# Performance work log

Measured on AMD Instinct MI355X. Metric: run time of the kernel, lower is better.

The kernel has to match this reference:

```python
import jax, jax.numpy as jnp
import numpy as np

B, C, Np, D = 16, 64, 128, 128
HT = 4      # time heads
HS = 4      # space heads (GAT)
F = D       # GAT out_channels
DK = D // 2 # q/k proj dim
TOPK = 8
NEG = -1e30

def ln(x, g, b):
    m = x.mean(-1, keepdims=True)
    v = jnp.mean((x - m) ** 2, axis=-1, keepdims=True)
    return (x - m) / jnp.sqrt(v + 1e-5) * g + b

def setup_inputs() -> dict:
    key = jax.random.key(0)
    ks = jax.random.split(key, 16)
    w = lambda k, s: (jax.random.normal(k, s, jnp.float32) * 0.02)
    return dict(
        H_in=jax.random.normal(ks[0], (B, C, Np, D), jnp.float32),
        static_adj=jax.random.normal(ks[1], (C, C), jnp.float32) * 0.1,
        attn_in_w=w(ks[2], (3 * D, D)), attn_in_b=jnp.zeros((3 * D,), jnp.float32),
        attn_out_w=w(ks[3], (D, D)), attn_out_b=jnp.zeros((D,), jnp.float32),
        ln1_g=jnp.ones((D,), jnp.float32), ln1_b=jnp.zeros((D,), jnp.float32),
        ln2_g=jnp.ones((D,), jnp.float32), ln2_b=jnp.zeros((D,), jnp.float32),
        ff1_w=w(ks[4], (4 * D, D)), ff1_b=jnp.zeros((4 * D,), jnp.float32),
        ff2_w=w(ks[5], (D, 4 * D)), ff2_b=jnp.zeros((D,), jnp.float32),
        tnorm_g=jnp.ones((D,), jnp.float32), tnorm_b=jnp.zeros((D,), jnp.float32),
        q_w=w(ks[6], (DK, D)), q_b=jnp.zeros((DK,), jnp.float32),
        k_w=w(ks[7], (DK, D)), k_b=jnp.zeros((DK,), jnp.float32),
        gat_w=w(ks[8], (HS, F, D)),
        gat_att_src=w(ks[9], (HS, F)), gat_att_dst=w(ks[10], (HS, F)),
        gat_bias=jnp.zeros((D,), jnp.float32),
        snorm_g=jnp.ones((D,), jnp.float32), snorm_b=jnp.zeros((D,), jnp.float32),
    )

def _forward(H_in, static_adj, attn_in_w, attn_in_b, attn_out_w, attn_out_b,
             ln1_g, ln1_b, ln2_g, ln2_b, ff1_w, ff1_b, ff2_w, ff2_b,
             tnorm_g, tnorm_b, q_w, q_b, k_w, k_b,
             gat_w, gat_att_src, gat_att_dst, gat_bias, snorm_g, snorm_b):
    dh = D // HT
    # ---- temporal transformer encoder layer (norm_first) on [B*C, Np, D]
    x0 = H_in.reshape(B * C, Np, D)
    h = ln(x0, ln1_g, ln1_b)
    qkv = h @ attn_in_w.T + attn_in_b
    q, k, v = jnp.split(qkv, 3, axis=-1)
    q = q.reshape(-1, Np, HT, dh).transpose(0, 2, 1, 3)
    k = k.reshape(-1, Np, HT, dh).transpose(0, 2, 1, 3)
    v = v.reshape(-1, Np, HT, dh).transpose(0, 2, 1, 3)
    att = jax.nn.softmax(jnp.einsum('nhqd,nhkd->nhqk', q, k) / jnp.sqrt(jnp.float32(dh)), axis=-1)
    o = jnp.einsum('nhqk,nhkd->nhqd', att, v).transpose(0, 2, 1, 3).reshape(-1, Np, D)
    x = x0 + (o @ attn_out_w.T + attn_out_b)
    h2 = ln(x, ln2_g, ln2_b)
    x = x + jax.nn.relu(h2 @ ff1_w.T + ff1_b) @ ff2_w.T + ff2_b
    H_temp = ln(x0 + x, tnorm_g, tnorm_b).reshape(B, C, Np, D)
    # ---- dynamic adjacency from temporal summary
    Hs = H_temp.mean(axis=2)                              # [B,C,D]
    q2 = Hs @ q_w.T + q_b
    k2 = Hs @ k_w.T + k_b
    sim = jnp.einsum('bcd,bed->bce', q2, k2) * (DK ** -0.5)
    A = jnp.tanh(sim) + static_adj[None]                  # [B,C,C]
    # ---- top-k edge mask per sample (row r -> its top-k cols, no self loops)
    kk = max(1, min(TOPK, C - 1))
    idx = jax.lax.top_k(A, kk)[1]                         # [B,C,kk]
    mask = jnp.any(jax.nn.one_hot(idx, C, dtype=bool), axis=2)  # [B,C,C]
    mask = mask & (~jnp.eye(C, dtype=bool)) & (A != 0)
    # ---- dense masked GAT over all (B, Np) graphs; src=row, dst=col
    xh = jnp.einsum('bcpd,hfd->bphcf', H_temp, gat_w)     # [B,Np,HS,C,F]
    asrc = jnp.einsum('bphcf,hf->bphc', xh, gat_att_src)
    adst = jnp.einsum('bphcf,hf->bphc', xh, gat_att_dst)
    e = asrc[..., :, None] + adst[..., None, :]           # [B,Np,HS,src,dst]
    e = jnp.where(e > 0, e, 0.2 * e)                      # LeakyReLU(0.2)
    mb = mask[:, None, None, :, :]
    e = jnp.where(mb, e, NEG)
    e = e - e.max(axis=3, keepdims=True)                  # softmax over src per dst
    wgt = jnp.exp(e) * mb
    s = wgt.sum(axis=3, keepdims=True)
    a = wgt / jnp.where(s > 0, s, 1.0)
    out = jnp.einsum('bphst,bphsf->bphtf', a, xh).mean(axis=2) + gat_bias  # [B,Np,C,F]
    out = out.transpose(0, 2, 1, 3)                       # [B,C,Np,D]
    return ln(out + H_temp, snorm_g, snorm_b)

def reference(H_in, static_adj, attn_in_w, attn_in_b, attn_out_w, attn_out_b,
              ln1_g, ln1_b, ln2_g, ln2_b, ff1_w, ff1_b, ff2_w, ff2_b,
              tnorm_g, tnorm_b, q_w, q_b, k_w, k_b,
              gat_w, gat_att_src, gat_att_dst, gat_bias, snorm_g, snorm_b):
    return _forward(H_in, static_adj, attn_in_w, attn_in_b, attn_out_w, attn_out_b,
                    ln1_g, ln1_b, ln2_g, ln2_b, ff1_w, ff1_b, ff2_w, ff2_b,
                    tnorm_g, tnorm_b, q_w, q_b, k_w, k_b,
                    gat_w, gat_att_src, gat_att_dst, gat_bias, snorm_g, snorm_b)
```

## Files before the change

kernel.cpp:

```cpp
#include <hip/hip_runtime.h>
#include <cstdint>


typedef __attribute__((ext_vector_type(8)))  short bf16x8;
typedef __attribute__((ext_vector_type(16))) float f32x16;
#define MFMA32(a, b, c) __builtin_amdgcn_mfma_f32_32x32x16_bf16((a), (b), (c), 0, 0, 0)

__device__ __forceinline__ unsigned short f2bf(float f) {
    unsigned int u = __float_as_uint(f);
    u += 0x7fffu + ((u >> 16) & 1u);
    return (unsigned short)(u >> 16);
}
__device__ __forceinline__ float bf2f(unsigned short u) {
    return __uint_as_float(((unsigned int)u) << 16);
}

__device__ __forceinline__ bf16x8 lds_frag(const unsigned short* p) {
    union { bf16x8 v; ushort4 h[2]; } u;
    u.h[0] = *(const ushort4*)p;
    u.h[1] = *(const ushort4*)(p + 4);
    return u.v;
}
__device__ __forceinline__ bf16x8 gfrag(const unsigned short* p) {
    union { bf16x8 v; uint4 u; } t;
    t.u = *(const uint4*)p;
    return t.v;
}

__device__ __forceinline__ int rowmap(int r, int hl) { return (r & 3) + 8 * (r >> 2) + 4 * hl; }

__global__ void wconv_kernel(const float* __restrict__ wqkv, const float* __restrict__ wout,
                             const float* __restrict__ w1, const float* __restrict__ w2,
                             const float* __restrict__ gw,
                             unsigned short* __restrict__ dst) {
    int i = blockIdx.x * 256 + threadIdx.x;
    float v;
    if (i < 49152)       v = wqkv[i];
    else if (i < 65536)  v = wout[i - 49152];
    else if (i < 131072) v = w1[i - 65536];
    else if (i < 196608) v = w2[i - 131072];
    else                 v = gw[i - 196608];
    dst[i] = f2bf(v);
}

__global__ void wa_kernel(const float* __restrict__ gw, const float* __restrict__ asw,
                          const float* __restrict__ adw,
                          float* __restrict__ waS, float* __restrict__ waD) {
    int t = blockIdx.x * 256 + threadIdx.x;
    int h = t >> 8, d = (t >> 1) & 127, which = t & 1;
    const float* av = which ? adw : asw;
    float s = 0.f;
    for (int f = 0; f < 128; f++) s += av[h * 128 + f] * gw[(h * 128 + f) * 128 + d];
    (which ? waD : waS)[h * 128 + d] = s;
}

__global__ __launch_bounds__(256, 1)
void seq_attn_kernel(const float* __restrict__ Hin,
                     const unsigned short* __restrict__ wqkv_b,
                     const float* __restrict__ bqkv,
                     const float* __restrict__ g1, const float* __restrict__ b1,
                     char* __restrict__ dout) {
    __shared__ unsigned short hb[128][132];
    __shared__ unsigned short qb[128][36];
    __shared__ unsigned short kb[128][36];
    __shared__ unsigned short vT[32][132];
    __shared__ unsigned short Bst[3][32][132];
    __shared__ unsigned short Pb[4][32][132];

    const int n = blockIdx.x;
    const int tid = threadIdx.x;
    const int lane = tid & 63;
    const int wv = tid >> 6;
    const int hl = lane >> 5;
    const int l31 = lane & 31;

    {
        int row = tid >> 1, hf = tid & 1;
        const float* src = Hin + ((long)n * 128 + row) * 128 + hf * 64;
        float xv[64];
        float s = 0.f, qs = 0.f;
#pragma unroll
        for (int i = 0; i < 64; i += 4) {
            float4 t = *(const float4*)(src + i);
            xv[i] = t.x; xv[i+1] = t.y; xv[i+2] = t.z; xv[i+3] = t.w;
        }
#pragma unroll
        for (int i = 0; i < 64; i++) { s += xv[i]; qs += xv[i] * xv[i]; }
        s += __shfl_xor(s, 1); qs += __shfl_xor(qs, 1);
        float mu = s * 0.0078125f;
        float rs = rsqrtf(fmaxf(qs * 0.0078125f - mu * mu, 0.f) + 1e-5f);
#pragma unroll
        for (int i = 0; i < 64; i++) {
            int d = hf * 64 + i;
            hb[row][d] = f2bf((xv[i] - mu) * rs * g1[d] + b1[d]);
        }
    }
    __syncthreads();

    unsigned short* Optr = (unsigned short*)(dout + (long)n * 65536 + 32768);

    for (int h = 0; h < 4; h++) {
        for (int idx = tid; idx < 1536; idx += 256) {
            int mat = idx >> 9;
            int rem = idx & 511;
            int j = rem >> 4, kc = rem & 15;
            const unsigned short* s8 = wqkv_b + ((mat * 128 + h * 32 + j) * 128 + kc * 8);
            ushort4 lo = *(const ushort4*)s8, hi = *(const ushort4*)(s8 + 4);
            unsigned short* d8 = &Bst[mat][j][kc * 8];
            *(ushort4*)d8 = lo; *(ushort4*)(d8 + 4) = hi;
        }
        __syncthreads();

        {
            f32x16 accq, acck, accv;
            float bq = bqkv[      h * 32 + l31];
            float bk = bqkv[128 + h * 32 + l31];
            float bv = bqkv[256 + h * 32 + l31];
#pragma unroll
            for (int r = 0; r < 16; r++) { accq[r] = bq; acck[r] = bk; accv[r] = bv; }
#pragma unroll
            for (int k0 = 0; k0 < 128; k0 += 16) {
                bf16x8 a  = lds_frag(&hb[wv * 32 + l31][k0 + hl * 8]);
                bf16x8 b0 = lds_frag(&Bst[0][l31][k0 + hl * 8]);
                bf16x8 b1f = lds_frag(&Bst[1][l31][k0 + hl * 8]);
                bf16x8 b2f = lds_frag(&Bst[2][l31][k0 + hl * 8]);
                accq = MFMA32(a, b0, accq);
                acck = MFMA32(a, b1f, acck);
                accv = MFMA32(a, b2f, accv);
            }
#pragma unroll
            for (int r = 0; r < 16; r++) {
                int tok = wv * 32 + rowmap(r, hl);
                qb[tok][l31] = f2bf(accq[r]);
                kb[tok][l31] = f2bf(acck[r]);
                vT[l31][tok] = f2bf(accv[r]);
            }
        }
        __syncthreads();

        f32x16 sacc[4];
#pragma unroll
        for (int t = 0; t < 4; t++)
#pragma unroll
            for (int r = 0; r < 16; r++) sacc[t][r] = 0.f;
#pragma unroll
        for (int k0 = 0; k0 < 32; k0 += 16) {
            bf16x8 a = lds_frag(&qb[wv * 32 + l31][k0 + hl * 8]);
#pragma unroll
            for (int t = 0; t < 4; t++) {
                bf16x8 b = lds_frag(&kb[t * 32 + l31][k0 + hl * 8]);
                sacc[t] = MFMA32(a, b, sacc[t]);
            }
        }
        const float scale = 0.17677669529663687f;
#pragma unroll
        for (int r = 0; r < 16; r++) {
            float m0 = fmaxf(fmaxf(sacc[0][r], sacc[1][r]), fmaxf(sacc[2][r], sacc[3][r]));
#pragma unroll
            for (int d = 1; d < 32; d <<= 1) m0 = fmaxf(m0, __shfl_xor(m0, d));
            float ssum = 0.f;
#pragma unroll
            for (int t = 0; t < 4; t++) {
                float e = __expf(scale * (sacc[t][r] - m0));
                sacc[t][r] = e; ssum += e;
            }
#pragma unroll
            for (int d = 1; d < 32; d <<= 1) ssum += __shfl_xor(ssum, d);
            float rinv = 1.f / ssum;
            int row = rowmap(r, hl);
#pragma unroll
            for (int t = 0; t < 4; t++)
                Pb[wv][row][t * 32 + l31] = f2bf(sacc[t][r] * rinv);
        }

        f32x16 oacc;
#pragma unroll
        for (int r = 0; r < 16; r++) oacc[r] = 0.f;
#pragma unroll
        for (int k0 = 0; k0 < 128; k0 += 16) {
            bf16x8 a = lds_frag(&Pb[wv][l31][k0 + hl * 8]);
            bf16x8 b = lds_frag(&vT[l31][k0 + hl * 8]);
            oacc = MFMA32(a, b, oacc);
        }
#pragma unroll
        for (int r = 0; r < 16; r++) {
            int tok = wv * 32 + rowmap(r, hl);
            Optr[tok * 128 + h * 32 + l31] = f2bf(oacc[r]);
        }
        __syncthreads();
    }
}

__global__ __launch_bounds__(256, 1)
void mlp_kernel(const float* __restrict__ Hin,
                const unsigned short* __restrict__ wout_b, const float* __restrict__ bout,
                const float* __restrict__ g2, const float* __restrict__ b2,
                const unsigned short* __restrict__ w1_b, const float* __restrict__ bf1,
                const unsigned short* __restrict__ w2_b, const float* __restrict__ bf2,
                const float* __restrict__ tg, const float* __restrict__ tb,
                char* __restrict__ dout) {
    __shared__ unsigned short Ab[128][132];
    __shared__ unsigned short h2b[128][132];
    __shared__ unsigned short BA[128][132];
    __shared__ unsigned short BB[128][132];

    const int n = blockIdx.x;
    const int tid = threadIdx.x;
    const int lane = tid & 63;
    const int wv = tid >> 6;
    const int hl = lane >> 5;
    const int l31 = lane & 31;

    const unsigned short* Optr = (const unsigned short*)(dout + (long)n * 65536 + 32768);

    for (int idx = tid; idx < 2048; idx += 256) {
        int row = idx >> 4, kc = idx & 15;
        {
            const ushort4* s = (const ushort4*)(Optr + row * 128 + kc * 8);
            unsigned short* d = &Ab[row][kc * 8];
            *(ushort4*)d = s[0]; *(ushort4*)(d + 4) = s[1];
        }
        {
            const ushort4* s = (const ushort4*)(wout_b + row * 128 + kc * 8);
            unsigned short* d = &BA[row][kc * 8];
            *(ushort4*)d = s[0]; *(ushort4*)(d + 4) = s[1];
        }
    }
    __syncthreads();

    f32x16 acc[4];
#pragma unroll
    for (int t = 0; t < 4; t++) {
        float bo = bout[t * 32 + l31];
#pragma unroll
        for (int r = 0; r < 16; r++) {
            int tok = wv * 32 + rowmap(r, hl);
            acc[t][r] = Hin[((long)n * 128 + tok) * 128 + t * 32 + l31] + bo;
        }
    }
#pragma unroll
    for (int k0 = 0; k0 < 128; k0 += 16) {
        bf16x8 a = lds_frag(&Ab[wv * 32 + l31][k0 + hl * 8]);
#pragma unroll
        for (int t = 0; t < 4; t++) {
            bf16x8 b = lds_frag(&BA[t * 32 + l31][k0 + hl * 8]);
            acc[t] = MFMA32(a, b, acc[t]);
        }
    }

#pragma unroll
    for (int r = 0; r < 16; r++) {
        float s = acc[0][r] + acc[1][r] + acc[2][r] + acc[3][r];
#pragma unroll
        for (int d = 1; d < 32; d <<= 1) s += __shfl_xor(s, d);
        float mu = s * 0.0078125f;
        float q = 0.f;
#pragma unroll
        for (int t = 0; t < 4; t++) { float dv = acc[t][r] - mu; q += dv * dv; }
#pragma unroll
        for (int d = 1; d < 32; d <<= 1) q += __shfl_xor(q, d);
        float rs = rsqrtf(q * 0.0078125f + 1e-5f);
        int row = wv * 32 + rowmap(r, hl);
#pragma unroll
        for (int t = 0; t < 4; t++) {
            int col = t * 32 + l31;
            h2b[row][col] = f2bf((acc[t][r] - mu) * rs * g2[col] + b2[col]);
        }
    }

    f32x16 acc2[4];
#pragma unroll
    for (int t = 0; t < 4; t++) {
        float bv = bf2[t * 32 + l31];
#pragma unroll
        for (int r = 0; r < 16; r++) acc2[t][r] = acc[t][r] + bv;
    }

    for (int j = 0; j < 4; j++) {
        __syncthreads();
        for (int idx = tid; idx < 2048; idx += 256) {
            int row = idx >> 4, kc = idx & 15;
            {
                const ushort4* s = (const ushort4*)(w1_b + ((j * 128 + row) * 128 + kc * 8));
                unsigned short* d = &BA[row][kc * 8];
                *(ushort4*)d = s[0]; *(ushort4*)(d + 4) = s[1];
            }
            {
                const ushort4* s = (const ushort4*)(w2_b + (row * 512 + j * 128 + kc * 8));
                unsigned short* d = &BB[row][kc * 8];
                *(ushort4*)d = s[0]; *(ushort4*)(d + 4) = s[1];
            }
        }
        __syncthreads();

        f32x16 racc[4];
#pragma unroll
        for (int t = 0; t < 4; t++) {
            float bv = bf1[j * 128 + t * 32 + l31];
#pragma unroll
            for (int r = 0; r < 16; r++) racc[t][r] = bv;
        }
#pragma unroll
        for (int k0 = 0; k0 < 128; k0 += 16) {
            bf16x8 a = lds_frag(&h2b[wv * 32 + l31][k0 + hl * 8]);
#pragma unroll
            for (int t = 0; t < 4; t++) {
                bf16x8 b = lds_frag(&BA[t * 32 + l31][k0 + hl * 8]);
                racc[t] = MFMA32(a, b, racc[t]);
            }
        }
#pragma unroll
        for (int t = 0; t < 4; t++)
#pragma unroll
            for (int r = 0; r < 16; r++) {
                int row = wv * 32 + rowmap(r, hl);
                Ab[row][t * 32 + l31] = f2bf(fmaxf(racc[t][r], 0.f));
            }

#pragma unroll
        for (int k0 = 0; k0 < 128; k0 += 16) {
            bf16x8 a = lds_frag(&Ab[wv * 32 + l31][k0 + hl * 8]);
#pragma unroll
            for (int t = 0; t < 4; t++) {
                bf16x8 b = lds_frag(&BB[t * 32 + l31][k0 + hl * 8]);
                acc2[t] = MFMA32(a, b, acc2[t]);
            }
        }
    }

#pragma unroll
    for (int t = 0; t < 4; t++)
#pragma unroll
        for (int r = 0; r < 16; r++) {
            int tok = wv * 32 + rowmap(r, hl);
            acc2[t][r] += Hin[((long)n * 128 + tok) * 128 + t * 32 + l31];
        }
    float* outf = (float*)dout + (long)n * 16384;
#pragma unroll
    for (int r = 0; r < 16; r++) {
        float s = acc2[0][r] + acc2[1][r] + acc2[2][r] + acc2[3][r];
#pragma unroll
        for (int d = 1; d < 32; d <<= 1) s += __shfl_xor(s, d);
        float mu = s * 0.0078125f;
        float q = 0.f;
#pragma unroll
        for (int t = 0; t < 4; t++) { float dv = acc2[t][r] - mu; q += dv * dv; }
#pragma unroll
        for (int d = 1; d < 32; d <<= 1) q += __shfl_xor(q, d);
        float rs = rsqrtf(q * 0.0078125f + 1e-5f);
        int tok = wv * 32 + rowmap(r, hl);
#pragma unroll
        for (int t = 0; t < 4; t++) {
            int col = t * 32 + l31;
            outf[tok * 128 + col] = (acc2[t][r] - mu) * rs * tg[col] + tb[col];
        }
    }
}

__global__ void hs_kernel(const float* __restrict__ Htemp, float* __restrict__ Hs) {
    int idx = blockIdx.x * 256 + threadIdx.x;
    int n = idx >> 7, d = idx & 127;
    float s = 0.f;
    for (int p = 0; p < 128; p++) s += Htemp[((long)n * 128 + p) * 128 + d];
    Hs[idx] = s * 0.0078125f;
}

__global__ __launch_bounds__(256)
void graph_kernel(const float* __restrict__ Hs,
                  const float* __restrict__ qw, const float* __restrict__ qb,
                  const float* __restrict__ kw, const float* __restrict__ kb,
                  const float* __restrict__ adj, unsigned long long* __restrict__ masks) {
    __shared__ float q2l[64][65];
    __shared__ float k2l[64][65];
    __shared__ float am[64][65];
    int b = blockIdx.x;
    int tid = threadIdx.x;
    {
        int r = tid & 127, jh = tid >> 7;
        int row = r & 63;
        const float* wmat = (r < 64) ? qw : kw;
        const float* bvec = (r < 64) ? qb : kb;
        const float* src = Hs + (long)(b * 64 + row) * 128;
        for (int jj = 0; jj < 32; jj++) {
            int j = jh * 32 + jj;
            const float* wrow = wmat + (long)j * 128;
            float s0 = 0.f, s1 = 0.f, s2 = 0.f, s3 = 0.f;
#pragma unroll
            for (int d = 0; d < 128; d += 4) {
                s0 += src[d] * wrow[d];     s1 += src[d+1] * wrow[d+1];
                s2 += src[d+2] * wrow[d+2]; s3 += src[d+3] * wrow[d+3];
            }
            float val = ((s0 + s1) + (s2 + s3)) + bvec[j];
            if (r < 64) q2l[row][j] = val; else k2l[row][j] = val;
        }
    }
    __syncthreads();
    {
        int c = tid & 63, eq = tid >> 6;
        for (int ee = 0; ee < 16; ee++) {
            int e = eq * 16 + ee;
            float s0 = 0.f, s1 = 0.f, s2 = 0.f, s3 = 0.f;
#pragma unroll
            for (int j = 0; j < 64; j += 4) {
                s0 += q2l[c][j]   * k2l[e][j];
                s1 += q2l[c][j+1] * k2l[e][j+1];
                s2 += q2l[c][j+2] * k2l[e][j+2];
                s3 += q2l[c][j+3] * k2l[e][j+3];
            }
            float sim = ((s0 + s1) + (s2 + s3)) * 0.125f;
            am[c][e] = tanhf(sim) + adj[c * 64 + e];
        }
    }
    __syncthreads();
    if (tid < 64) {
        int c = tid;
        unsigned long long sel = 0ull;
        for (int it = 0; it < 8; it++) {
            float best = -1e38f; int bi = 0;
            for (int e = 0; e < 64; e++) {
                float v = am[c][e];
                bool ok = (((sel >> e) & 1ull) == 0ull) && (v > best);
                best = ok ? v : best;
                bi = ok ? e : bi;
            }
            sel |= (1ull << bi);
        }
        sel &= ~(1ull << c);
        for (int e = 0; e < 64; e++)
            if (am[c][e] == 0.f) sel &= ~(1ull << e);
        masks[b * 64 + c] = sel;
    }
}

__global__ __launch_bounds__(256, 1)
void gat_kernel(float* __restrict__ Htemp,
                const unsigned short* __restrict__ gwb,
                const float* __restrict__ waS, const float* __restrict__ waD,
                const float* __restrict__ gbias,
                const unsigned long long* __restrict__ masks,
                const float* __restrict__ sg, const float* __restrict__ sb) {
    __shared__ unsigned short Htb[64][132];
    __shared__ double ovl_d[3264];
    __shared__ float asrcF[4][64], adstF[4][64];
    __shared__ float pmax[4][64], psum[4][64];
    __shared__ unsigned long long mk[64];

    unsigned short (*xhT)[68]  = (unsigned short(*)[68])ovl_d;
    unsigned short (*attT)[68] = (unsigned short(*)[68])((char*)ovl_d + 17408);
    float (*part)[8][64]       = (float(*)[8][64])ovl_d;

    const int bp = blockIdx.x;
    const int b = bp >> 7, p = bp & 127;
    const int tid = threadIdx.x;
    const int lane = tid & 63, wv = tid >> 6;
    const int hl = lane >> 5, l31 = lane & 31;
    const int rs = (wv & 1) * 32;
    const int cs = (wv >> 1) * 64;

    {
        int c = tid >> 2, qq = tid & 3;
        const float* src = Htemp + ((long)(b * 64 + c) * 128 + p) * 128 + qq * 32;
#pragma unroll
        for (int k = 0; k < 8; k++) {
            float4 t4 = *(const float4*)(src + 4 * k);
            ushort4 u; u.x = f2bf(t4.x); u.y = f2bf(t4.y); u.z = f2bf(t4.z); u.w = f2bf(t4.w);
            *(ushort4*)&Htb[c][qq * 32 + 4 * k] = u;
        }
    }
    if (tid < 64) mk[tid] = masks[b * 64 + tid];
    __syncthreads();

    {
        int s = lane, q = wv;
        float acc[8];
#pragma unroll
        for (int m = 0; m < 8; m++) acc[m] = 0.f;
        const unsigned int* hp = (const unsigned int*)&Htb[s][q * 32];
#pragma unroll
        for (int d2 = 0; d2 < 16; d2++) {
            unsigned int u = hp[d2];
            float f0 = __uint_as_float(u << 16);
            float f1 = __uint_as_float(u & 0xffff0000u);
            int d = q * 32 + 2 * d2;
#pragma unroll
            for (int h = 0; h < 4; h++) {
                acc[2*h]   += f0 * waS[h * 128 + d] + f1 * waS[h * 128 + d + 1];
                acc[2*h+1] += f0 * waD[h * 128 + d] + f1 * waD[h * 128 + d + 1];
            }
        }
#pragma unroll
        for (int m = 0; m < 8; m++) part[q][m][s] = acc[m];
    }
    __syncthreads();
    for (int o = tid; o < 512; o += 256) {
        int h = o >> 7, rem = o & 127, which = rem >> 6, s = rem & 63;
        int m = h * 2 + which;
        float v = part[0][m][s] + part[1][m][s] + part[2][m][s] + part[3][m][s];
        if (which == 0) asrcF[h][s] = v; else adstF[h][s] = v;
    }
    __syncthreads();

    f32x16 oacc0, oacc1;
#pragma unroll
    for (int r = 0; r < 16; r++) { oacc0[r] = 0.f; oacc1[r] = 0.f; }

    for (int h = 0; h < 4; h++) {
        f32x16 a0, a1;
#pragma unroll
        for (int r = 0; r < 16; r++) { a0[r] = 0.f; a1[r] = 0.f; }
        const unsigned short* gwh = gwb + h * 16384;
#pragma unroll
        for (int k0 = 0; k0 < 128; k0 += 16) {
            bf16x8 af = lds_frag(&Htb[rs + l31][k0 + hl * 8]);
            bf16x8 b0 = gfrag(gwh + (cs + l31) * 128 + k0 + hl * 8);
            bf16x8 b1 = gfrag(gwh + (cs + 32 + l31) * 128 + k0 + hl * 8);
            a0 = MFMA32(af, b0, a0);
            a1 = MFMA32(af, b1, a1);
        }
#pragma unroll
        for (int g = 0; g < 4; g++) {
            ushort4 u0, u1;
            u0.x = f2bf(a0[4*g]);   u0.y = f2bf(a0[4*g+1]);
            u0.z = f2bf(a0[4*g+2]); u0.w = f2bf(a0[4*g+3]);
            u1.x = f2bf(a1[4*g]);   u1.y = f2bf(a1[4*g+1]);
            u1.z = f2bf(a1[4*g+2]); u1.w = f2bf(a1[4*g+3]);
            int so = rs + 4 * hl + 8 * g;
            *(ushort4*)&xhT[cs + l31][so]      = u0;
            *(ushort4*)&xhT[cs + 32 + l31][so] = u1;
        }
        __syncthreads();

        {
            int t = lane;
            float adv = adstF[h][t];
            float ev[16];
            float mx = -1e30f;
#pragma unroll
            for (int i = 0; i < 16; i++) {
                int s = wv * 16 + i;
                float e = asrcF[h][s] + adv;
                e = (e > 0.f) ? e : 0.2f * e;
                ev[i] = e;
                if ((mk[s] >> t) & 1ull) mx = fmaxf(mx, e);
            }
            pmax[wv][t] = mx;
            __syncthreads();
            float M = fmaxf(fmaxf(pmax[0][t], pmax[1][t]), fmaxf(pmax[2][t], pmax[3][t]));
            float sm = 0.f;
#pragma unroll
            for (int i = 0; i < 16; i++) {
                int s = wv * 16 + i;
                float w = ((mk[s] >> t) & 1ull) ? __expf(ev[i] - M) : 0.f;
                ev[i] = w; sm += w;
            }
            psum[wv][t] = sm;
            __syncthreads();
            float S = psum[0][t] + psum[1][t] + psum[2][t] + psum[3][t];
            float rinv = (S > 0.f) ? 1.f / S : 0.f;
#pragma unroll
            for (int g = 0; g < 4; g++) {
                ushort4 u;
                u.x = f2bf(ev[4*g]   * rinv); u.y = f2bf(ev[4*g+1] * rinv);
                u.z = f2bf(ev[4*g+2] * rinv); u.w = f2bf(ev[4*g+3] * rinv);
                *(ushort4*)&attT[t][wv * 16 + 4 * g] = u;
            }
        }
        __syncthreads();

#pragma unroll
        for (int k0 = 0; k0 < 64; k0 += 16) {
            bf16x8 af = lds_frag(&attT[rs + l31][k0 + hl * 8]);
            bf16x8 b0 = lds_frag(&xhT[cs + l31][k0 + hl * 8]);
            bf16x8 b1 = lds_frag(&xhT[cs + 32 + l31][k0 + hl * 8]);
            oacc0 = MFMA32(af, b0, oacc0);
            oacc1 = MFMA32(af, b1, oacc1);
        }
        __syncthreads();
    }

    float gb0 = gbias[cs + l31], gb1 = gbias[cs + 32 + l31];
    float v0[16], v1[16];
#pragma unroll
    for (int r = 0; r < 16; r++) {
        int c = rs + rowmap(r, hl);
        v0[r] = oacc0[r] * 0.25f + gb0 + bf2f(Htb[c][cs + l31]);
        v1[r] = oacc1[r] * 0.25f + gb1 + bf2f(Htb[c][cs + 32 + l31]);
    }
#pragma unroll
    for (int r = 0; r < 16; r++) {
        float s = v0[r] + v1[r];
        float q = v0[r] * v0[r] + v1[r] * v1[r];
#pragma unroll
        for (int d = 1; d < 32; d <<= 1) { s += __shfl_xor(s, d); q += __shfl_xor(q, d); }
        if (l31 == 0) {
            int c = rs + rowmap(r, hl);
            pmax[wv >> 1][c] = s;
            psum[wv >> 1][c] = q;
        }
    }
    __syncthreads();
    float sgv0 = sg[cs + l31], sbv0 = sb[cs + l31];
    float sgv1 = sg[cs + 32 + l31], sbv1 = sb[cs + 32 + l31];
#pragma unroll
    for (int r = 0; r < 16; r++) {
        int c = rs + rowmap(r, hl);
        float sum = pmax[0][c] + pmax[1][c];
        float sq  = psum[0][c] + psum[1][c];
        float mu = sum * 0.0078125f;
        float var = sq * 0.0078125f - mu * mu;
        float rsd = rsqrtf(fmaxf(var, 0.f) + 1e-5f);
        float* orow = Htemp + ((long)(b * 64 + c) * 128 + p) * 128;
        orow[cs + l31]      = (v0[r] - mu) * rsd * sgv0 + sbv0;
        orow[cs + 32 + l31] = (v1[r] - mu) * rsd * sgv1 + sbv1;
    }
}

extern "C" void kernel_launch(void* const* d_in, const int* in_sizes, int n_in,
                              void* d_out, int out_size, void* d_ws, size_t ws_size,
                              hipStream_t stream) {
    const float* Hin        = (const float*)d_in[0];
    const float* static_adj = (const float*)d_in[1];
    const float* attn_in_w  = (const float*)d_in[2];
    const float* attn_in_b  = (const float*)d_in[3];
    const float* attn_out_w = (const float*)d_in[4];
    const float* attn_out_b = (const float*)d_in[5];
    const float* ln1_g      = (const float*)d_in[6];
    const float* ln1_b      = (const float*)d_in[7];
    const float* ln2_g      = (const float*)d_in[8];
    const float* ln2_b      = (const float*)d_in[9];
    const float* ff1_w      = (const float*)d_in[10];
    const float* ff1_b      = (const float*)d_in[11];
    const float* ff2_w      = (const float*)d_in[12];
    const float* ff2_b      = (const float*)d_in[13];
    const float* tnorm_g    = (const float*)d_in[14];
    const float* tnorm_b    = (const float*)d_in[15];
    const float* q_w        = (const float*)d_in[16];
    const float* q_b        = (const float*)d_in[17];
    const float* k_w        = (const float*)d_in[18];
    const float* k_b        = (const float*)d_in[19];
    const float* gat_w      = (const float*)d_in[20];
    const float* gat_att_src= (const float*)d_in[21];
    const float* gat_att_dst= (const float*)d_in[22];
    const float* gat_bias   = (const float*)d_in[23];
    const float* snorm_g    = (const float*)d_in[24];
    const float* snorm_b    = (const float*)d_in[25];

    char* out = (char*)d_out;
    char* ws = (char*)d_ws;
    unsigned short* wb = (unsigned short*)ws;
    const unsigned short* wqkv_b = wb;
    const unsigned short* wout_b = wb + 49152;
    const unsigned short* w1_b   = wb + 65536;
    const unsigned short* w2_b   = wb + 131072;
    const unsigned short* gw_b   = wb + 196608;
    unsigned long long* masks = (unsigned long long*)(ws + 524288);
    float* Hs  = (float*)(ws + 532480);
    float* waS = (float*)(ws + 1056768);
    float* waD = (float*)(ws + 1058816);

    hipLaunchKernelGGL(wconv_kernel, dim3(1024), dim3(256), 0, stream,
                       attn_in_w, attn_out_w, ff1_w, ff2_w, gat_w, wb);
    hipLaunchKernelGGL(wa_kernel, dim3(4), dim3(256), 0, stream,
                       gat_w, gat_att_src, gat_att_dst, waS, waD);
    hipLaunchKernelGGL(seq_attn_kernel, dim3(1024), dim3(256), 0, stream,
                       Hin, wqkv_b, attn_in_b, ln1_g, ln1_b, out);
    hipLaunchKernelGGL(mlp_kernel, dim3(1024), dim3(256), 0, stream,
                       Hin, wout_b, attn_out_b, ln2_g, ln2_b,
                       w1_b, ff1_b, w2_b, ff2_b, tnorm_g, tnorm_b, out);
    hipLaunchKernelGGL(hs_kernel, dim3(512), dim3(256), 0, stream, (float*)out, Hs);
    hipLaunchKernelGGL(graph_kernel, dim3(16), dim3(256), 0, stream,
                       Hs, q_w, q_b, k_w, k_b, static_adj, masks);
    hipLaunchKernelGGL(gat_kernel, dim3(2048), dim3(256), 0, stream,
                       (float*)out, gw_b, waS, waD, gat_bias,
                       masks, snorm_g, snorm_b);
}
```

Measured before the change: 657.4 us.

## Fuse temporal attention and MLP into one kernel with global-read weight fragments

Result: faster. 622.9 us (-5.2%).

```diff
diff --git a/kernel.cpp b/kernel.cpp
--- a/kernel.cpp
+++ b/kernel.cpp
@@ -54,18 +54,23 @@
     (which ? waD : waS)[h * 128 + d] = s;
 }
 
-__global__ __launch_bounds__(256, 1)
-void seq_attn_kernel(const float* __restrict__ Hin,
-                     const unsigned short* __restrict__ wqkv_b,
-                     const float* __restrict__ bqkv,
+__global__ __launch_bounds__(256, 2)
+void temporal_kernel(const float* __restrict__ Hin,
+                     const unsigned short* __restrict__ wqkv_b, const float* __restrict__ bqkv,
+                     const unsigned short* __restrict__ wout_b, const float* __restrict__ bout,
                      const float* __restrict__ g1, const float* __restrict__ b1,
-                     char* __restrict__ dout) {
-    __shared__ unsigned short hb[128][132];
-    __shared__ unsigned short qb[128][36];
-    __shared__ unsigned short kb[128][36];
-    __shared__ unsigned short vT[32][132];
-    __shared__ unsigned short Bst[3][32][132];
-    __shared__ unsigned short Pb[4][32][132];
+                     const float* __restrict__ g2, const float* __restrict__ b2,
+                     const unsigned short* __restrict__ w1_b, const float* __restrict__ bf1,
+                     const unsigned short* __restrict__ w2_b, const float* __restrict__ bf2,
+                     const float* __restrict__ tg, const float* __restrict__ tb,
+                     float* __restrict__ Htemp) {
+    __shared__ unsigned short RA[128][132];
+    __shared__ double RBd[4512];
+    unsigned short (*qb)[36]  = (unsigned short(*)[36])RBd;
+    unsigned short (*kb)[36]  = (unsigned short(*)[36])((char*)RBd + 9216);
+    unsigned short (*vT)[132] = (unsigned short(*)[132])((char*)RBd + 18432);
+    unsigned short (*Pb)[36]  = (unsigned short(*)[36])((char*)RBd + 26880);
+    unsigned short (*h2b)[132] = (unsigned short(*)[132])RBd;
 
     const int n = blockIdx.x;
     const int tid = threadIdx.x;
@@ -73,6 +78,7 @@
     const int wv = tid >> 6;
     const int hl = lane >> 5;
     const int l31 = lane & 31;
+    const int myrow = wv * 32 + l31;
 
     {
         int row = tid >> 1, hf = tid & 1;
@@ -92,25 +98,17 @@
 #pragma unroll
         for (int i = 0; i < 64; i++) {
             int d = hf * 64 + i;
-            hb[row][d] = f2bf((xv[i] - mu) * rs * g1[d] + b1[d]);
-        }
-    }
-    __syncthreads();
-
-    unsigned short* Optr = (unsigned short*)(dout + (long)n * 65536 + 32768);
+            RA[row][d] = f2bf((xv[i] - mu) * rs * g1[d] + b1[d]);
+        }
+    }
+
+    f32x16 oaccH[4];
+#pragma unroll
+    for (int h = 0; h < 4; h++)
+#pragma unroll
+        for (int r = 0; r < 16; r++) oaccH[h][r] = 0.f;
 
     for (int h = 0; h < 4; h++) {
-        for (int idx = tid; idx < 1536; idx += 256) {
-            int mat = idx >> 9;
-            int rem = idx & 511;
-            int j = rem >> 4, kc = rem & 15;
-            const unsigned short* s8 = wqkv_b + ((mat * 128 + h * 32 + j) * 128 + kc * 8);
-            ushort4 lo = *(const ushort4*)s8, hi = *(const ushort4*)(s8 + 4);
-            unsigned short* d8 = &Bst[mat][j][kc * 8];
-            *(ushort4*)d8 = lo; *(ushort4*)(d8 + 4) = hi;
-        }
-        __syncthreads();
-
         {
             f32x16 accq, acck, accv;
             float bq = bqkv[      h * 32 + l31];
@@ -118,15 +116,15 @@
             float bv = bqkv[256 + h * 32 + l31];
 #pragma unroll
             for (int r = 0; r < 16; r++) { accq[r] = bq; acck[r] = bk; accv[r] = bv; }
+            const unsigned short* wq = wqkv_b + (      h * 32 + l31) * 128 + hl * 8;
+            const unsigned short* wk = wqkv_b + (128 + h * 32 + l31) * 128 + hl * 8;
+            const unsigned short* wvp= wqkv_b + (256 + h * 32 + l31) * 128 + hl * 8;
 #pragma unroll
             for (int k0 = 0; k0 < 128; k0 += 16) {
-                bf16x8 a  = lds_frag(&hb[wv * 32 + l31][k0 + hl * 8]);
-                bf16x8 b0 = lds_frag(&Bst[0][l31][k0 + hl * 8]);
-                bf16x8 b1f = lds_frag(&Bst[1][l31][k0 + hl * 8]);
-                bf16x8 b2f = lds_frag(&Bst[2][l31][k0 + hl * 8]);
-                accq = MFMA32(a, b0, accq);
-                acck = MFMA32(a, b1f, acck);
-                accv = MFMA32(a, b2f, accv);
+                bf16x8 a  = lds_frag(&RA[myrow][k0 + hl * 8]);
+                accq = MFMA32(a, gfrag(wq + k0), accq);
+                acck = MFMA32(a, gfrag(wk + k0), acck);
+                accv = MFMA32(a, gfrag(wvp + k0), accv);
             }
 #pragma unroll
             for (int r = 0; r < 16; r++) {
@@ -145,7 +143,7 @@
             for (int r = 0; r < 16; r++) sacc[t][r] = 0.f;
 #pragma unroll
         for (int k0 = 0; k0 < 32; k0 += 16) {
-            bf16x8 a = lds_frag(&qb[wv * 32 + l31][k0 + hl * 8]);
+            bf16x8 a = lds_frag(&qb[myrow][k0 + hl * 8]);
 #pragma unroll
             for (int t = 0; t < 4; t++) {
                 bf16x8 b = lds_frag(&kb[t * 32 + l31][k0 + hl * 8]);
@@ -167,66 +165,32 @@
 #pragma unroll
             for (int d = 1; d < 32; d <<= 1) ssum += __shfl_xor(ssum, d);
             float rinv = 1.f / ssum;
-            int row = rowmap(r, hl);
-#pragma unroll
-            for (int t = 0; t < 4; t++)
-                Pb[wv][row][t * 32 + l31] = f2bf(sacc[t][r] * rinv);
-        }
-
-        f32x16 oacc;
-#pragma unroll
-        for (int r = 0; r < 16; r++) oacc[r] = 0.f;
-#pragma unroll
-        for (int k0 = 0; k0 < 128; k0 += 16) {
-            bf16x8 a = lds_frag(&Pb[wv][l31][k0 + hl * 8]);
-            bf16x8 b = lds_frag(&vT[l31][k0 + hl * 8]);
-            oacc = MFMA32(a, b, oacc);
-        }
+#pragma unroll
+            for (int t = 0; t < 4; t++) sacc[t][r] *= rinv;
+        }
+
+#pragma unroll
+        for (int t = 0; t < 4; t++) {
+#pragma unroll
+            for (int r = 0; r < 16; r++)
+                Pb[wv * 32 + rowmap(r, hl)][l31] = f2bf(sacc[t][r]);
+#pragma unroll
+            for (int k0 = 0; k0 < 32; k0 += 16) {
+                bf16x8 a = lds_frag(&Pb[wv * 32 + l31][k0 + hl * 8]);
+                bf16x8 b = lds_frag(&vT[l31][t * 32 + k0 + hl * 8]);
+                oaccH[h] = MFMA32(a, b, oaccH[h]);
+            }
+        }
+        __syncthreads();
+    }
+
+#pragma unroll
+    for (int h = 0; h < 4; h++)
 #pragma unroll
         for (int r = 0; r < 16; r++) {
             int tok = wv * 32 + rowmap(r, hl);
-            Optr[tok * 128 + h * 32 + l31] = f2bf(oacc[r]);
-        }
-        __syncthreads();
-    }
-}
-
-__global__ __launch_bounds__(256, 1)
-void mlp_kernel(const float* __restrict__ Hin,
-                const unsigned short* __restrict__ wout_b, const float* __restrict__ bout,
-                const float* __restrict__ g2, const float* __restrict__ b2,
-                const unsigned short* __restrict__ w1_b, const float* __restrict__ bf1,
-                const unsigned short* __restrict__ w2_b, const float* __restrict__ bf2,
-                const float* __restrict__ tg, const float* __restrict__ tb,
-                char* __restrict__ dout) {
-    __shared__ unsigned short Ab[128][132];
-    __shared__ unsigned short h2b[128][132];
-    __shared__ unsigned short BA[128][132];
-    __shared__ unsigned short BB[128][132];
-
-    const int n = blockIdx.x;
-    const int tid = threadIdx.x;
-    const int lane = tid & 63;
-    const int wv = tid >> 6;
-    const int hl = lane >> 5;
-    const int l31 = lane & 31;
-
-    const unsigned short* Optr = (const unsigned short*)(dout + (long)n * 65536 + 32768);
-
-    for (int idx = tid; idx < 2048; idx += 256) {
-        int row = idx >> 4, kc = idx & 15;
-        {
-            const ushort4* s = (const ushort4*)(Optr + row * 128 + kc * 8);
-            unsigned short* d = &Ab[row][kc * 8];
-            *(ushort4*)d = s[0]; *(ushort4*)(d + 4) = s[1];
-        }
-        {
-            const ushort4* s = (const ushort4*)(wout_b + row * 128 + kc * 8);
-            unsigned short* d = &BA[row][kc * 8];
-            *(ushort4*)d = s[0]; *(ushort4*)(d + 4) = s[1];
-        }
-    }
-    __syncthreads();
+            RA[tok][h * 32 + l31] = f2bf(oaccH[h][r]);
+        }
 
     f32x16 acc[4];
 #pragma unroll
@@ -240,10 +204,10 @@
     }
 #pragma unroll
     for (int k0 = 0; k0 < 128; k0 += 16) {
-        bf16x8 a = lds_frag(&Ab[wv * 32 + l31][k0 + hl * 8]);
+        bf16x8 a = lds_frag(&RA[myrow][k0 + hl * 8]);
 #pragma unroll
         for (int t = 0; t < 4; t++) {
-            bf16x8 b = lds_frag(&BA[t * 32 + l31][k0 + hl * 8]);
+            bf16x8 b = gfrag(wout_b + (t * 32 + l31) * 128 + k0 + hl * 8);
             acc[t] = MFMA32(a, b, acc[t]);
         }
     }
@@ -277,22 +241,6 @@
     }
 
     for (int j = 0; j < 4; j++) {
-        __syncthreads();
-        for (int idx = tid; idx < 2048; idx += 256) {
-            int row = idx >> 4, kc = idx & 15;
-            {
-                const ushort4* s = (const ushort4*)(w1_b + ((j * 128 + row) * 128 + kc * 8));
-                unsigned short* d = &BA[row][kc * 8];
-                *(ushort4*)d = s[0]; *(ushort4*)(d + 4) = s[1];
-            }
-            {
-                const ushort4* s = (const ushort4*)(w2_b + (row * 512 + j * 128 + kc * 8));
-                unsigned short* d = &BB[row][kc * 8];
-                *(ushort4*)d = s[0]; *(ushort4*)(d + 4) = s[1];
-            }
-        }
-        __syncthreads();
-
         f32x16 racc[4];
 #pragma unroll
         for (int t = 0; t < 4; t++) {
@@ -302,10 +250,10 @@
         }
 #pragma unroll
         for (int k0 = 0; k0 < 128; k0 += 16) {
-            bf16x8 a = lds_frag(&h2b[wv * 32 + l31][k0 + hl * 8]);
+            bf16x8 a = lds_frag(&h2b[myrow][k0 + hl * 8]);
 #pragma unroll
             for (int t = 0; t < 4; t++) {
-                bf16x8 b = lds_frag(&BA[t * 32 + l31][k0 + hl * 8]);
+                bf16x8 b = gfrag(w1_b + (j * 128 + t * 32 + l31) * 128 + k0 + hl * 8);
                 racc[t] = MFMA32(a, b, racc[t]);
             }
         }
@@ -314,15 +262,14 @@
 #pragma unroll
             for (int r = 0; r < 16; r++) {
                 int row = wv * 32 + rowmap(r, hl);
-                Ab[row][t * 32 + l31] = f2bf(fmaxf(racc[t][r], 0.f));
-            }
-
+                RA[row][t * 32 + l31] = f2bf(fmaxf(racc[t][r], 0.f));
+            }
 #pragma unroll
         for (int k0 = 0; k0 < 128; k0 += 16) {
-            bf16x8 a = lds_frag(&Ab[wv * 32 + l31][k0 + hl * 8]);
+            bf16x8 a = lds_frag(&RA[myrow][k0 + hl * 8]);
 #pragma unroll
             for (int t = 0; t < 4; t++) {
-                bf16x8 b = lds_frag(&BB[t * 32 + l31][k0 + hl * 8]);
+                bf16x8 b = gfrag(w2_b + (t * 32 + l31) * 512 + j * 128 + k0 + hl * 8);
                 acc2[t] = MFMA32(a, b, acc2[t]);
             }
         }
@@ -335,7 +282,7 @@
             int tok = wv * 32 + rowmap(r, hl);
             acc2[t][r] += Hin[((long)n * 128 + tok) * 128 + t * 32 + l31];
         }
-    float* outf = (float*)dout + (long)n * 16384;
+    float* outf = Htemp + (long)n * 16384;
 #pragma unroll
     for (int r = 0; r < 16; r++) {
         float s = acc2[0][r] + acc2[1][r] + acc2[2][r] + acc2[3][r];
@@ -645,7 +592,7 @@
     const float* snorm_g    = (const float*)d_in[24];
     const float* snorm_b    = (const float*)d_in[25];
 
-    char* out = (char*)d_out;
+    float* out = (float*)d_out;
     char* ws = (char*)d_ws;
     unsigned short* wb = (unsigned short*)ws;
     const unsigned short* wqkv_b = wb;
@@ -662,15 +609,14 @@
                        attn_in_w, attn_out_w, ff1_w, ff2_w, gat_w, wb);
     hipLaunchKernelGGL(wa_kernel, dim3(4), dim3(256), 0, stream,
                        gat_w, gat_att_src, gat_att_dst, waS, waD);
-    hipLaunchKernelGGL(seq_attn_kernel, dim3(1024), dim3(256), 0, stream,
-                       Hin, wqkv_b, attn_in_b, ln1_g, ln1_b, out);
-    hipLaunchKernelGGL(mlp_kernel, dim3(1024), dim3(256), 0, stream,
-                       Hin, wout_b, attn_out_b, ln2_g, ln2_b,
+    hipLaunchKernelGGL(temporal_kernel, dim3(1024), dim3(256), 0, stream,
+                       Hin, wqkv_b, attn_in_b, wout_b, attn_out_b,
+                       ln1_g, ln1_b, ln2_g, ln2_b,
                        w1_b, ff1_b, w2_b, ff2_b, tnorm_g, tnorm_b, out);
-    hipLaunchKernelGGL(hs_kernel, dim3(512), dim3(256), 0, stream, (float*)out, Hs);
+    hipLaunchKernelGGL(hs_kernel, dim3(512), dim3(256), 0, stream, out, Hs);
     hipLaunchKernelGGL(graph_kernel, dim3(16), dim3(256), 0, stream,
                        Hs, q_w, q_b, k_w, k_b, static_adj, masks);
     hipLaunchKernelGGL(gat_kernel, dim3(2048), dim3(256), 0, stream,
-                       (float*)out, gw_b, waS, waD, gat_bias,
+                       out, gw_b, waS, waD, gat_bias,
                        masks, snorm_g, snorm_b);
 }
```
